# Performance work log

Hardware: AMD Instinct MI355X
Metric: run time of the kernel (lower is better)

Reference implementation:

```python
import jax, jax.numpy as jnp
import numpy as np


def _pairwise_sq_dist(a, b):
    # a: (B,N,D), b: (B,M,D) -> (B,N,M) squared euclidean distances
    # matmul trick matching torch.cdist (clamped at 0 before implicit sqrt)
    a2 = jnp.sum(a * a, axis=-1)  # (B,N)
    b2 = jnp.sum(b * b, axis=-1)  # (B,M)
    ab = jnp.einsum('bnd,bmd->bnm', a, b)  # (B,N,M)
    d2 = a2[:, :, None] + b2[:, None, :] - 2.0 * ab
    return jnp.maximum(d2, 0.0)


def setup_inputs() -> dict:
    key = jax.random.key(0)
    k1, k2 = jax.random.split(key)
    B, N, M, D = 8, 8192, 8192, 3
    gts = jax.random.normal(k1, (B, N, D), dtype=jnp.float32)
    preds = jax.random.normal(k2, (B, M, D), dtype=jnp.float32)
    return {"gts": gts, "preds": preds}


def reference(gts, preds):
    d2 = _pairwise_sq_dist(gts, preds)           # (B,N,M)
    min_g2p = jnp.min(d2, axis=2)                # (B,N) nearest pred for each gt
    min_p2g = jnp.min(d2, axis=1)                # (B,M) nearest gt for each pred
    return jnp.mean(min_g2p) + jnp.mean(min_p2g)
```

## Files before the change

### kernel.cpp

```cpp
#include <hip/hip_runtime.h>
#include <math.h>


#define BB 8
#define NPTS 8192
#define ROWS 512
#define CH 1024
#define NPAIR (CH / 64)

typedef __attribute__((ext_vector_type(8)))  short short8;
typedef __attribute__((ext_vector_type(16))) float float16;

#define ONE_BF16 ((short)0x3F80)

__device__ inline unsigned short bf16rn(float f) {
    unsigned int u = __float_as_uint(f);
    u += 0x7FFFu + ((u >> 16) & 1u);
    return (unsigned short)(u >> 16);
}
__device__ inline float bf2f(unsigned short h) {
    return __uint_as_float(((unsigned int)h) << 16);
}
__device__ inline float min3f(float a, float b, float c) {
    return fminf(fminf(a, b), c);
}
__device__ inline float min16(const float16 d) {
    float t0 = min3f(d[0],  d[1],  d[2]);
    float t1 = min3f(d[3],  d[4],  d[5]);
    float t2 = min3f(d[6],  d[7],  d[8]);
    float t3 = min3f(d[9],  d[10], d[11]);
    float t4 = min3f(d[12], d[13], d[14]);
    return fminf(min3f(t0, t1, t2), min3f(t3, t4, d[15]));
}

#define DPP_FMIN(v, CTRL) do {                                                \
    int _s = __builtin_amdgcn_update_dpp(__float_as_int(v), __float_as_int(v),\
                                         (CTRL), 0xf, 0xf, false);            \
    (v) = fminf((v), __int_as_float(_s)); } while (0)

__device__ inline void packB(float x, float y, float z, short8& lo, short8& hi) {
    float w = x * x + y * y + z * z;
    unsigned short xh = bf16rn(x), yh = bf16rn(y), zh = bf16rn(z);
    unsigned short xl = bf16rn(x - bf2f(xh));
    unsigned short yl = bf16rn(y - bf2f(yh));
    unsigned short zl = bf16rn(z - bf2f(zh));
    unsigned short wh = bf16rn(w), wl = bf16rn(w - bf2f(wh));
    lo[0]=(short)xh; lo[1]=(short)yh; lo[2]=(short)zh; lo[3]=(short)xl;
    lo[4]=(short)yl; lo[5]=(short)zl; lo[6]=(short)xh; lo[7]=(short)yh;
    hi[0]=(short)zh; hi[1]=ONE_BF16;  hi[2]=ONE_BF16;  hi[3]=(short)wh;
    hi[4]=(short)wl; hi[5]=0;         hi[6]=0;         hi[7]=0;
}
__device__ inline void packA(float x, float y, float z, short8& lo, short8& hi) {
    float w = x * x + y * y + z * z;
    float mx = -2.0f * x, my = -2.0f * y, mz = -2.0f * z;
    unsigned short xh = bf16rn(mx), yh = bf16rn(my), zh = bf16rn(mz);
    unsigned short xl = bf16rn(mx - bf2f(xh));
    unsigned short yl = bf16rn(my - bf2f(yh));
    unsigned short zl = bf16rn(mz - bf2f(zh));
    unsigned short wh = bf16rn(w), wl = bf16rn(w - bf2f(wh));
    lo[0]=(short)xh; lo[1]=(short)yh; lo[2]=(short)zh; lo[3]=(short)xh;
    lo[4]=(short)yh; lo[5]=(short)zh; lo[6]=(short)xl; lo[7]=(short)yl;
    hi[0]=(short)zl; hi[1]=(short)wh; hi[2]=(short)wl; hi[3]=ONE_BF16;
    hi[4]=ONE_BF16;  hi[5]=0;         hi[6]=0;         hi[7]=0;
}

__global__ __launch_bounds__(512, 4) void chamfer_main(
    const float* __restrict__ gts, const float* __restrict__ preds,
    unsigned int* __restrict__ minn, unsigned int* __restrict__ minp)
{
    __shared__ short8 sB[2][CH];
    __shared__ int colmin[CH];

    const int b       = blockIdx.z;
    const int rowBase = blockIdx.x * ROWS;
    const int colBase = blockIdx.y * CH;
    const int tid  = threadIdx.x;
    const int lane = tid & 63;
    const int wave = tid >> 6;
    const int h    = lane >> 5;
    const int c    = lane & 31;

    for (int i = tid; i < CH; i += 512) {
        const float* p = preds + ((size_t)b * NPTS + colBase + i) * 3;
        short8 lo, hi;
        packB(p[0], p[1], p[2], lo, hi);
        sB[0][i] = lo; sB[1][i] = hi;
        colmin[i] = 0x7F800000;
    }

    short8 a[2];
    {
        const float* g = gts + ((size_t)b * NPTS + rowBase + wave * 64 + c) * 3;
#pragma unroll
        for (int r = 0; r < 2; ++r) {
            short8 lo, hi;
            packA(g[r*96], g[r*96+1], g[r*96+2], lo, hi);
            a[r] = h ? hi : lo;
        }
    }

    float16 zacc;
#pragma unroll
    for (int q = 0; q < 16; ++q) zacc[q] = 0.0f;

    const float kInf = __builtin_inff();
    float rm[2][16];
#pragma unroll
    for (int r = 0; r < 2; ++r)
#pragma unroll
        for (int q = 0; q < 16; ++q) rm[r][q] = kInf;

    __syncthreads();

    const short8* myB = &sB[h][c];

#pragma unroll 2
    for (int tp = 0; tp < NPAIR; ++tp) {
        short8 b0 = myB[tp * 64];
        short8 b1 = myB[tp * 64 + 32];
        float16 d0 = __builtin_amdgcn_mfma_f32_32x32x16_bf16(a[0], b0, zacc, 0, 0, 0);
        float16 d1 = __builtin_amdgcn_mfma_f32_32x32x16_bf16(a[0], b1, zacc, 0, 0, 0);
#pragma unroll
        for (int q = 0; q < 16; ++q) rm[0][q] = min3f(rm[0][q], d0[q], d1[q]);
        float c0 = min16(d0);
        float c1 = min16(d1);
        d0 = __builtin_amdgcn_mfma_f32_32x32x16_bf16(a[1], b0, zacc, 0, 0, 0);
        d1 = __builtin_amdgcn_mfma_f32_32x32x16_bf16(a[1], b1, zacc, 0, 0, 0);
#pragma unroll
        for (int q = 0; q < 16; ++q) rm[1][q] = min3f(rm[1][q], d0[q], d1[q]);
        c0 = fminf(c0, min16(d0));
        c1 = fminf(c1, min16(d1));
        c0 = fminf(c0, __shfl_xor(c0, 32));
        c1 = fminf(c1, __shfl_xor(c1, 32));
        float cv = h ? c1 : c0;
        atomicMin(&colmin[tp * 64 + lane], __float_as_int(cv));
    }

#pragma unroll
    for (int r = 0; r < 2; ++r)
#pragma unroll
        for (int q = 0; q < 16; ++q) {
            float v = rm[r][q];
            DPP_FMIN(v, 0x111);
            DPP_FMIN(v, 0x112);
            DPP_FMIN(v, 0x114);
            DPP_FMIN(v, 0x118);
            DPP_FMIN(v, 0x142);
            rm[r][q] = v;
        }
    if ((lane & 31) == 31) {
        unsigned int* mb = minn + (size_t)b * NPTS + rowBase + wave * 64;
#pragma unroll
        for (int r = 0; r < 2; ++r)
#pragma unroll
            for (int q = 0; q < 16; ++q) {
                int row = r * 32 + (q & 3) + 8 * (q >> 2) + 4 * h;
                atomicMin(&mb[row], __float_as_uint(fmaxf(rm[r][q], 0.0f)));
            }
    }

    __syncthreads();
    unsigned int* minp_b = minp + (size_t)b * NPTS + colBase;
    for (int i = tid; i < CH; i += 512) {
        unsigned int bits = __float_as_uint(fmaxf(__int_as_float(colmin[i]), 0.0f));
        atomicMin(&minp_b[i], bits);
    }
}

__global__ void chamfer_reduce(const unsigned int* __restrict__ minn,
                               const unsigned int* __restrict__ minp,
                               float* __restrict__ accum,
                               unsigned int* __restrict__ ticket,
                               float* __restrict__ out)
{
    const int idx = blockIdx.x * blockDim.x + threadIdx.x;
    const int stride = gridDim.x * blockDim.x;

    float s0 = 0.0f, s1 = 0.0f;
    for (int i = idx; i < BB * NPTS; i += stride) s0 += __uint_as_float(minn[i]);
    for (int i = idx; i < BB * NPTS; i += stride) s1 += __uint_as_float(minp[i]);

#pragma unroll
    for (int m = 1; m < 64; m <<= 1) {
        s0 += __shfl_xor(s0, m, 64);
        s1 += __shfl_xor(s1, m, 64);
    }
    __shared__ float w0[4], w1[4];
    if ((threadIdx.x & 63) == 0) {
        w0[threadIdx.x >> 6] = s0;
        w1[threadIdx.x >> 6] = s1;
    }
    __syncthreads();
    if (threadIdx.x == 0) {
        atomicAdd(&accum[0], w0[0] + w0[1] + w0[2] + w0[3]);
        atomicAdd(&accum[1], w1[0] + w1[1] + w1[2] + w1[3]);
        __threadfence();
        unsigned int old = atomicAdd(ticket, 1u);
        unsigned int G = gridDim.x;
        if (old == 0xAAAAAAAAu + G - 1u || old == G - 1u) {
            float a0 = atomicAdd(&accum[0], 0.0f);
            float a1 = atomicAdd(&accum[1], 0.0f);
            out[0] = a0 / (float)(BB * NPTS) + a1 / (float)(BB * NPTS);
        }
    }
}

extern "C" void kernel_launch(void* const* d_in, const int* in_sizes, int n_in,
                              void* d_out, int out_size, void* d_ws, size_t ws_size,
                              hipStream_t stream) {
    const float* gts   = (const float*)d_in[0];
    const float* preds = (const float*)d_in[1];
    float* out = (float*)d_out;

    unsigned int* minn   = (unsigned int*)d_ws;
    unsigned int* minp   = minn + (size_t)BB * NPTS;
    float*        accum  = (float*)(minp + (size_t)BB * NPTS);
    unsigned int* ticket = (unsigned int*)(accum + 2);

    dim3 grid(NPTS / ROWS, NPTS / CH, BB);
    chamfer_main<<<grid, 512, 0, stream>>>(gts, preds, minn, minp);

    chamfer_reduce<<<64, 256, 0, stream>>>(minn, minp, accum, ticket, out);
}
```

Measured before the change: 95.60 us.

## Halve rows per block, use one A fragment per wave, prefetch B tiles

Each wave now handles 32 gt rows instead of 64, so ROWS drops to 256 and the grid doubles in x. The per-tile column reduction drops the cross-half shuffle and issues two LDS atomicMins per lane, one per 32-column half, instead of one. B fragments for the next iteration are loaded from LDS one step ahead to hide LDS latency. This cuts per-thread register use and doubles the block count, at the cost of reloading and repacking B per block and issuing more LDS and global atomics per MFMA.

```diff
diff --git a/kernel.cpp b/kernel.cpp
--- a/kernel.cpp
+++ b/kernel.cpp
@@ -4,7 +4,7 @@
 
 #define BB 8
 #define NPTS 8192
-#define ROWS 512
+#define ROWS 256
 #define CH 1024
 #define NPAIR (CH / 64)
 
@@ -88,15 +88,12 @@
         colmin[i] = 0x7F800000;
     }
 
-    short8 a[2];
+    short8 afrag;
     {
-        const float* g = gts + ((size_t)b * NPTS + rowBase + wave * 64 + c) * 3;
-#pragma unroll
-        for (int r = 0; r < 2; ++r) {
-            short8 lo, hi;
-            packA(g[r*96], g[r*96+1], g[r*96+2], lo, hi);
-            a[r] = h ? hi : lo;
-        }
+        const float* g = gts + ((size_t)b * NPTS + rowBase + wave * 32 + c) * 3;
+        short8 lo, hi;
+        packA(g[0], g[1], g[2], lo, hi);
+        afrag = h ? hi : lo;
     }
 
     float16 zacc;
@@ -104,59 +101,48 @@
     for (int q = 0; q < 16; ++q) zacc[q] = 0.0f;
 
     const float kInf = __builtin_inff();
-    float rm[2][16];
-#pragma unroll
-    for (int r = 0; r < 2; ++r)
-#pragma unroll
-        for (int q = 0; q < 16; ++q) rm[r][q] = kInf;
+    float rm[16];
+#pragma unroll
+    for (int q = 0; q < 16; ++q) rm[q] = kInf;
 
     __syncthreads();
 
     const short8* myB = &sB[h][c];
 
+    short8 nb0 = myB[0];
+    short8 nb1 = myB[32];
 #pragma unroll 2
     for (int tp = 0; tp < NPAIR; ++tp) {
-        short8 b0 = myB[tp * 64];
-        short8 b1 = myB[tp * 64 + 32];
-        float16 d0 = __builtin_amdgcn_mfma_f32_32x32x16_bf16(a[0], b0, zacc, 0, 0, 0);
-        float16 d1 = __builtin_amdgcn_mfma_f32_32x32x16_bf16(a[0], b1, zacc, 0, 0, 0);
-#pragma unroll
-        for (int q = 0; q < 16; ++q) rm[0][q] = min3f(rm[0][q], d0[q], d1[q]);
-        float c0 = min16(d0);
-        float c1 = min16(d1);
-        d0 = __builtin_amdgcn_mfma_f32_32x32x16_bf16(a[1], b0, zacc, 0, 0, 0);
-        d1 = __builtin_amdgcn_mfma_f32_32x32x16_bf16(a[1], b1, zacc, 0, 0, 0);
-#pragma unroll
-        for (int q = 0; q < 16; ++q) rm[1][q] = min3f(rm[1][q], d0[q], d1[q]);
-        c0 = fminf(c0, min16(d0));
-        c1 = fminf(c1, min16(d1));
-        c0 = fminf(c0, __shfl_xor(c0, 32));
-        c1 = fminf(c1, __shfl_xor(c1, 32));
-        float cv = h ? c1 : c0;
-        atomicMin(&colmin[tp * 64 + lane], __float_as_int(cv));
-    }
-
-#pragma unroll
-    for (int r = 0; r < 2; ++r)
+        short8 b0 = nb0, b1 = nb1;
+        if (tp + 1 < NPAIR) {
+            nb0 = myB[(tp + 1) * 64];
+            nb1 = myB[(tp + 1) * 64 + 32];
+        }
+        float16 d0 = __builtin_amdgcn_mfma_f32_32x32x16_bf16(afrag, b0, zacc, 0, 0, 0);
+        float16 d1 = __builtin_amdgcn_mfma_f32_32x32x16_bf16(afrag, b1, zacc, 0, 0, 0);
+#pragma unroll
+        for (int q = 0; q < 16; ++q) rm[q] = min3f(rm[q], d0[q], d1[q]);
+        atomicMin(&colmin[tp * 64 + c],      __float_as_int(min16(d0)));
+        atomicMin(&colmin[tp * 64 + 32 + c], __float_as_int(min16(d1)));
+    }
+
+#pragma unroll
+    for (int q = 0; q < 16; ++q) {
+        float v = rm[q];
+        DPP_FMIN(v, 0x111);
+        DPP_FMIN(v, 0x112);
+        DPP_FMIN(v, 0x114);
+        DPP_FMIN(v, 0x118);
+        DPP_FMIN(v, 0x142);
+        rm[q] = v;
+    }
+    if ((lane & 31) == 31) {
+        unsigned int* mb = minn + (size_t)b * NPTS + rowBase + wave * 32;
 #pragma unroll
         for (int q = 0; q < 16; ++q) {
-            float v = rm[r][q];
-            DPP_FMIN(v, 0x111);
-            DPP_FMIN(v, 0x112);
-            DPP_FMIN(v, 0x114);
-            DPP_FMIN(v, 0x118);
-            DPP_FMIN(v, 0x142);
-            rm[r][q] = v;
+            int row = (q & 3) + 8 * (q >> 2) + 4 * h;
+            atomicMin(&mb[row], __float_as_uint(fmaxf(rm[q], 0.0f)));
         }
-    if ((lane & 31) == 31) {
-        unsigned int* mb = minn + (size_t)b * NPTS + rowBase + wave * 64;
-#pragma unroll
-        for (int r = 0; r < 2; ++r)
-#pragma unroll
-            for (int q = 0; q < 16; ++q) {
-                int row = r * 32 + (q & 3) + 8 * (q >> 2) + 4 * h;
-                atomicMin(&mb[row], __float_as_uint(fmaxf(rm[r][q], 0.0f)));
-            }
     }
 
     __syncthreads();
```

Result: slower. 100.7 us (+5.3%).
